# Optimization experiments

Measured on AMD Instinct MI355X. Metric: run time of the kernel, lower is better.

## Reference

```python
import jax, jax.numpy as jnp
import numpy as np

B, S, D = 8, 2048, 256


def setup_inputs() -> dict:
    key = jax.random.key(0)
    k1, k2, k3, k4, k5 = jax.random.split(key, 5)
    head = jax.random.normal(k1, (B, S, D), dtype=jnp.float32)
    dep = jax.random.normal(k2, (B, S, D), dtype=jnp.float32)
    edge_U = jax.random.normal(k3, (D, D), dtype=jnp.float32) / np.sqrt(D)
    edge_W = jax.random.normal(k4, (1, 2 * D), dtype=jnp.float32) / np.sqrt(2 * D)
    edge_b = jax.random.normal(k5, (1,), dtype=jnp.float32)
    return {"head": head, "dep": dep, "edge_U": edge_U, "edge_W": edge_W, "edge_b": edge_b}


def reference(head, dep, edge_U, edge_W, edge_b):
    # t1[b,i,o] = head[b,i,:] @ U @ dep[b,o,:]  -> [B,S,S]
    t1 = jnp.einsum('bid,de,boe->bio', head, edge_U, dep)
    # t2: linear over pairwise concat(head_i, dep_o); decomposes into two
    # broadcast-added matvecs (same math as W @ concat, no [B,S^2,2D] tensor).
    d = head.shape[-1]
    wh, wd = edge_W[0, :d], edge_W[0, d:]
    hs = head @ wh  # [B,S]
    ds = dep @ wd   # [B,S]
    t2 = hs[:, :, None] + ds[:, None, :]  # [B,S,S]
    return t1 + t2 + edge_b[0]
```

## Files before the change

kernel.cpp:

```cpp
#include <hip/hip_runtime.h>
#include <hip/hip_bf16.h>
#include <stdint.h>
#include <stddef.h>

#define B_ 8
#define S_ 2048
#define D_ 256
#define NROWS (B_ * S_)

typedef __attribute__((ext_vector_type(8))) short short8;
typedef __attribute__((ext_vector_type(4))) short short4v;
typedef __attribute__((ext_vector_type(4))) float f32x4;

__device__ __forceinline__ short bf16of(float f) {
  union { float f; unsigned u; } x; x.f = f;
  unsigned r = x.u + 0x7FFFu + ((x.u >> 16) & 1u);
  return (short)(r >> 16);
}

__device__ __forceinline__ void async_ld16(const void* g, void* s) {
  __builtin_amdgcn_global_load_lds(
      (const __attribute__((address_space(1))) void*)g,
      (__attribute__((address_space(3))) void*)s, 16, 0, 0);
}

__global__ void k_prep_u(const float* __restrict__ U, short* __restrict__ UT) {
  int n = blockIdx.x;
  int k = threadIdx.x;
  UT[n * D_ + k] = bf16of(U[k * D_ + n]);
}

__global__ void k_rows(const float* __restrict__ head, const float* __restrict__ dep,
                       const float* __restrict__ W,
                       float* __restrict__ hs, float* __restrict__ ds,
                       short* __restrict__ headB, short* __restrict__ depB) {
  const float* X; const float* wv; float* sv; short* XB;
  if (blockIdx.y == 0) { X = head; wv = W;      sv = hs; XB = headB; }
  else                 { X = dep;  wv = W + D_; sv = ds; XB = depB;  }
  const int row = blockIdx.x * 4 + (threadIdx.x >> 6);
  const int l = threadIdx.x & 63;
  const float4 v  = *(const float4*)(X + (size_t)row * D_ + l * 4);
  const float4 wq = *(const float4*)(wv + l * 4);
  short4v pk;
  pk[0] = bf16of(v.x); pk[1] = bf16of(v.y); pk[2] = bf16of(v.z); pk[3] = bf16of(v.w);
  *(short4v*)(XB + (size_t)row * D_ + l * 4) = pk;
  float p = v.x * wq.x + v.y * wq.y + v.z * wq.z + v.w * wq.w;
  p += __shfl_xor(p, 1); p += __shfl_xor(p, 2); p += __shfl_xor(p, 4);
  p += __shfl_xor(p, 8); p += __shfl_xor(p, 16); p += __shfl_xor(p, 32);
  if (l == 0) sv[row] = p;
}

__launch_bounds__(256, 2)
__global__ void k_ahat(const short* __restrict__ headB, const short* __restrict__ UT,
                       short* __restrict__ Ahat) {
  __shared__ __align__(16) short sU[4 * 128 * 32];
  __shared__ __align__(16) short sH[4 * 128 * 32];
  const int t = threadIdx.x;
  const int w = t >> 6;
  const int l = t & 63;
  const int quad = l >> 4;
  const int nbase = blockIdx.x * 128;
  const int mbase = blockIdx.y * 128;

  f32x4 acc[4][4];
#pragma unroll
  for (int i = 0; i < 4; ++i)
#pragma unroll
    for (int j = 0; j < 4; ++j) acc[i][j] = (f32x4)0.0f;

  for (int it = 0; it < 2; ++it) {
    __syncthreads();
#pragma unroll
    for (int kb = 0; kb < 4; ++kb) {
#pragma unroll
      for (int c = 0; c < 2; ++c) {
        int q = c * 256 + t;
        int r = q >> 2, qc = q & 3;
        int kk = it * 128 + kb * 32 + qc * 8;
        async_ld16(UT + (size_t)(nbase + r) * D_ + kk, (char*)sU + kb * 8192 + q * 16);
        async_ld16(headB + (size_t)(mbase + r) * D_ + kk, (char*)sH + kb * 8192 + q * 16);
      }
    }
    __syncthreads();
    const short8* pU = (const short8*)sU;
    const short8* pH = (const short8*)sH;
#pragma unroll
    for (int kb = 0; kb < 4; ++kb) {
      short8 aF[4], bF[4];
#pragma unroll
      for (int mt = 0; mt < 4; ++mt)
        aF[mt] = pU[(kb * 128 + (w >> 1) * 64 + mt * 16 + (l & 15)) * 4 + quad];
#pragma unroll
      for (int nt = 0; nt < 4; ++nt)
        bF[nt] = pH[(kb * 128 + (w & 1) * 64 + nt * 16 + (l & 15)) * 4 + quad];
#pragma unroll
      for (int mt = 0; mt < 4; ++mt)
#pragma unroll
        for (int nt = 0; nt < 4; ++nt)
          acc[mt][nt] = __builtin_amdgcn_mfma_f32_16x16x32_bf16(aF[mt], bF[nt], acc[mt][nt], 0, 0, 0);
    }
  }

#pragma unroll
  for (int mt = 0; mt < 4; ++mt) {
    int n_loc = (w >> 1) * 64 + mt * 16 + quad * 4;
#pragma unroll
    for (int nt = 0; nt < 4; ++nt) {
      int i_loc = (w & 1) * 64 + nt * 16 + (l & 15);
      short4v pk;
      pk[0] = bf16of(acc[mt][nt][0]); pk[1] = bf16of(acc[mt][nt][1]);
      pk[2] = bf16of(acc[mt][nt][2]); pk[3] = bf16of(acc[mt][nt][3]);
      *(short4v*)(Ahat + (size_t)(mbase + i_loc) * D_ + nbase + n_loc) = pk;
    }
  }
}

__launch_bounds__(256, 3)
__global__ void k_main(const short* __restrict__ Ahat, const short* __restrict__ depB,
                       const float* __restrict__ hs, const float* __restrict__ ds,
                       const float* __restrict__ eb, float* __restrict__ out) {
  __shared__ __align__(16) short sA[2 * 128 * 32];
  __shared__ __align__(16) short sD[2 * 128 * 32];
  __shared__ float hs_s[128];
  __shared__ float ds_s[128];
  const int t = threadIdx.x;
  const int w = t >> 6;
  const int l = t & 63;
  const int quad = l >> 4;
  const int b = blockIdx.z;
  const int mbase = blockIdx.y * 128;
  const int nbase = blockIdx.x * 128;

  if (t < 128) hs_s[t] = hs[b * S_ + mbase + t];
  else         ds_s[t - 128] = ds[b * S_ + nbase + t - 128];

  f32x4 acc[4][4];
#pragma unroll
  for (int i = 0; i < 4; ++i)
#pragma unroll
    for (int j = 0; j < 4; ++j) acc[i][j] = (f32x4)0.0f;

  for (int it = 0; it < 4; ++it) {
    __syncthreads();
#pragma unroll
    for (int kb = 0; kb < 2; ++kb) {
#pragma unroll
      for (int c = 0; c < 2; ++c) {
        int q = c * 256 + t;
        int r = q >> 2, qc = q & 3;
        int kk = it * 64 + kb * 32 + qc * 8;
        async_ld16(Ahat + (size_t)(b * S_ + mbase + r) * D_ + kk, (char*)sA + kb * 8192 + q * 16);
        async_ld16(depB + (size_t)(b * S_ + nbase + r) * D_ + kk, (char*)sD + kb * 8192 + q * 16);
      }
    }
    __syncthreads();
    const short8* pA = (const short8*)sA;
    const short8* pD = (const short8*)sD;
#pragma unroll
    for (int kb = 0; kb < 2; ++kb) {
      short8 aF[4], bF[4];
#pragma unroll
      for (int mt = 0; mt < 4; ++mt)
        aF[mt] = pD[(kb * 128 + (w >> 1) * 64 + mt * 16 + (l & 15)) * 4 + quad];
#pragma unroll
      for (int nt = 0; nt < 4; ++nt)
        bF[nt] = pA[(kb * 128 + (w & 1) * 64 + nt * 16 + (l & 15)) * 4 + quad];
#pragma unroll
      for (int mt = 0; mt < 4; ++mt)
#pragma unroll
        for (int nt = 0; nt < 4; ++nt)
          acc[mt][nt] = __builtin_amdgcn_mfma_f32_16x16x32_bf16(aF[mt], bF[nt], acc[mt][nt], 0, 0, 0);
    }
  }

  const float bias = eb[0];
#pragma unroll
  for (int mt = 0; mt < 4; ++mt) {
    int o_loc = (w >> 1) * 64 + mt * 16 + quad * 4;
    float4 dsv = *(const float4*)&ds_s[o_loc];
#pragma unroll
    for (int nt = 0; nt < 4; ++nt) {
      int i_loc = (w & 1) * 64 + nt * 16 + (l & 15);
      float hv = hs_s[i_loc] + bias;
      f32x4 a = acc[mt][nt];
      float4 o4;
      o4.x = a[0] + hv + dsv.x;
      o4.y = a[1] + hv + dsv.y;
      o4.z = a[2] + hv + dsv.z;
      o4.w = a[3] + hv + dsv.w;
      *(float4*)(out + (size_t)(b * S_ + mbase + i_loc) * S_ + nbase + o_loc) = o4;
    }
  }
}

extern "C" void kernel_launch(void* const* d_in, const int* in_sizes, int n_in,
                              void* d_out, int out_size, void* d_ws, size_t ws_size,
                              hipStream_t stream) {
  const float* head = (const float*)d_in[0];
  const float* dep  = (const float*)d_in[1];
  const float* U    = (const float*)d_in[2];
  const float* W    = (const float*)d_in[3];
  const float* eb   = (const float*)d_in[4];
  float* out = (float*)d_out;

  char* ws = (char*)d_ws;
  short* UT    = (short*)ws;
  float* hs    = (float*)(ws + (128 << 10));
  float* ds    = (float*)(ws + (192 << 10));
  short* headB = (short*)(ws + (256 << 10));
  short* depB  = (short*)(ws + (256 << 10) + (8 << 20));
  short* Ahat  = (short*)(ws + (256 << 10) + (16 << 20));

  k_prep_u<<<dim3(256), dim3(256), 0, stream>>>(U, UT);
  k_rows<<<dim3(NROWS / 4, 2), dim3(256), 0, stream>>>(head, dep, W, hs, ds, headB, depB);
  k_ahat<<<dim3(2, 128), dim3(256), 0, stream>>>(headB, UT, Ahat);
  k_main<<<dim3(16, 16, 8), dim3(256), 0, stream>>>(Ahat, depB, hs, ds, eb, out);
}
```

Baseline: 193.4 us.

## Load MFMA fragments directly from global memory instead of staging through LDS

Both GEMM kernels drop their LDS staging buffers and barriers. Each wave now loads its bf16 MFMA operand fragments straight from global memory (16-byte vector loads per lane) inside a K loop unrolled by two. The epilogue bias vectors are also read directly from global memory rather than shared memory, and k_ahat's occupancy hint goes from 2 to 3. This removes LDS traffic and synchronisation, but operands are no longer shared across the waves of a block, so each tile is fetched redundantly from L1/L2 with strided access.

```diff
diff --git a/kernel.cpp b/kernel.cpp
--- a/kernel.cpp
+++ b/kernel.cpp
@@ -16,12 +16,6 @@
   union { float f; unsigned u; } x; x.f = f;
   unsigned r = x.u + 0x7FFFu + ((x.u >> 16) & 1u);
   return (short)(r >> 16);
-}
-
-__device__ __forceinline__ void async_ld16(const void* g, void* s) {
-  __builtin_amdgcn_global_load_lds(
-      (const __attribute__((address_space(1))) void*)g,
-      (__attribute__((address_space(3))) void*)s, 16, 0, 0);
 }
 
 __global__ void k_prep_u(const float* __restrict__ U, short* __restrict__ UT) {
@@ -50,17 +44,19 @@
   if (l == 0) sv[row] = p;
 }
 
-__launch_bounds__(256, 2)
+__launch_bounds__(256, 3)
 __global__ void k_ahat(const short* __restrict__ headB, const short* __restrict__ UT,
                        short* __restrict__ Ahat) {
-  __shared__ __align__(16) short sU[4 * 128 * 32];
-  __shared__ __align__(16) short sH[4 * 128 * 32];
   const int t = threadIdx.x;
   const int w = t >> 6;
   const int l = t & 63;
   const int quad = l >> 4;
+  const int r15 = l & 15;
   const int nbase = blockIdx.x * 128;
   const int mbase = blockIdx.y * 128;
+
+  const short* pA = UT + (size_t)(nbase + (w >> 1) * 64 + r15) * D_ + quad * 8;
+  const short* pB = headB + (size_t)(mbase + (w & 1) * 64 + r15) * D_ + quad * 8;
 
   f32x4 acc[4][4];
 #pragma unroll
@@ -68,37 +64,20 @@
 #pragma unroll
     for (int j = 0; j < 4; ++j) acc[i][j] = (f32x4)0.0f;
 
-  for (int it = 0; it < 2; ++it) {
-    __syncthreads();
+#pragma unroll 2
+  for (int k0 = 0; k0 < D_; k0 += 32) {
+    short8 aF[4], bF[4];
 #pragma unroll
-    for (int kb = 0; kb < 4; ++kb) {
+    for (int mt = 0; mt < 4; ++mt)
+      aF[mt] = *(const short8*)(pA + (size_t)(mt * 16) * D_ + k0);
 #pragma unroll
-      for (int c = 0; c < 2; ++c) {
-        int q = c * 256 + t;
-        int r = q >> 2, qc = q & 3;
-        int kk = it * 128 + kb * 32 + qc * 8;
-        async_ld16(UT + (size_t)(nbase + r) * D_ + kk, (char*)sU + kb * 8192 + q * 16);
-        async_ld16(headB + (size_t)(mbase + r) * D_ + kk, (char*)sH + kb * 8192 + q * 16);
-      }
-    }
-    __syncthreads();
-    const short8* pU = (const short8*)sU;
-    const short8* pH = (const short8*)sH;
+    for (int nt = 0; nt < 4; ++nt)
+      bF[nt] = *(const short8*)(pB + (size_t)(nt * 16) * D_ + k0);
 #pragma unroll
-    for (int kb = 0; kb < 4; ++kb) {
-      short8 aF[4], bF[4];
-#pragma unroll
-      for (int mt = 0; mt < 4; ++mt)
-        aF[mt] = pU[(kb * 128 + (w >> 1) * 64 + mt * 16 + (l & 15)) * 4 + quad];
+    for (int mt = 0; mt < 4; ++mt)
 #pragma unroll
       for (int nt = 0; nt < 4; ++nt)
-        bF[nt] = pH[(kb * 128 + (w & 1) * 64 + nt * 16 + (l & 15)) * 4 + quad];
-#pragma unroll
-      for (int mt = 0; mt < 4; ++mt)
-#pragma unroll
-        for (int nt = 0; nt < 4; ++nt)
-          acc[mt][nt] = __builtin_amdgcn_mfma_f32_16x16x32_bf16(aF[mt], bF[nt], acc[mt][nt], 0, 0, 0);
-    }
+        acc[mt][nt] = __builtin_amdgcn_mfma_f32_16x16x32_bf16(aF[mt], bF[nt], acc[mt][nt], 0, 0, 0);
   }
 
 #pragma unroll
@@ -106,7 +85,7 @@
     int n_loc = (w >> 1) * 64 + mt * 16 + quad * 4;
 #pragma unroll
     for (int nt = 0; nt < 4; ++nt) {
-      int i_loc = (w & 1) * 64 + nt * 16 + (l & 15);
+      int i_loc = (w & 1) * 64 + nt * 16 + r15;
       short4v pk;
       pk[0] = bf16of(acc[mt][nt][0]); pk[1] = bf16of(acc[mt][nt][1]);
       pk[2] = bf16of(acc[mt][nt][2]); pk[3] = bf16of(acc[mt][nt][3]);
@@ -119,20 +98,17 @@
 __global__ void k_main(const short* __restrict__ Ahat, const short* __restrict__ depB,
                        const float* __restrict__ hs, const float* __restrict__ ds,
                        const float* __restrict__ eb, float* __restrict__ out) {
-  __shared__ __align__(16) short sA[2 * 128 * 32];
-  __shared__ __align__(16) short sD[2 * 128 * 32];
-  __shared__ float hs_s[128];
-  __shared__ float ds_s[128];
   const int t = threadIdx.x;
   const int w = t >> 6;
   const int l = t & 63;
   const int quad = l >> 4;
+  const int r15 = l & 15;
   const int b = blockIdx.z;
   const int mbase = blockIdx.y * 128;
   const int nbase = blockIdx.x * 128;
 
-  if (t < 128) hs_s[t] = hs[b * S_ + mbase + t];
-  else         ds_s[t - 128] = ds[b * S_ + nbase + t - 128];
+  const short* pA = depB + (size_t)(b * S_ + nbase + (w >> 1) * 64 + r15) * D_ + quad * 8;
+  const short* pB = Ahat + (size_t)(b * S_ + mbase + (w & 1) * 64 + r15) * D_ + quad * 8;
 
   f32x4 acc[4][4];
 #pragma unroll
@@ -140,48 +116,36 @@
 #pragma unroll
     for (int j = 0; j < 4; ++j) acc[i][j] = (f32x4)0.0f;
 
-  for (int it = 0; it < 4; ++it) {
-    __syncthreads();
+#pragma unroll 2
+  for (int k0 = 0; k0 < D_; k0 += 32) {
+    short8 aF[4], bF[4];
 #pragma unroll
-    for (int kb = 0; kb < 2; ++kb) {
+    for (int mt = 0; mt < 4; ++mt)
+      aF[mt] = *(const short8*)(pA + (size_t)(mt * 16) * D_ + k0);
 #pragma unroll
-      for (int c = 0; c < 2; ++c) {
-        int q = c * 256 + t;
-        int r = q >> 2, qc = q & 3;
-        int kk = it * 64 + kb * 32 + qc * 8;
-        async_ld16(Ahat + (size_t)(b * S_ + mbase + r) * D_ + kk, (char*)sA + kb * 8192 + q * 16);
-        async_ld16(depB + (size_t)(b * S_ + nbase + r) * D_ + kk, (char*)sD + kb * 8192 + q * 16);
-      }
-    }
-    __syncthreads();
-    const short8* pA = (const short8*)sA;
-    const short8* pD = (const short8*)sD;
+    for (int nt = 0; nt < 4; ++nt)
+      bF[nt] = *(const short8*)(pB + (size_t)(nt * 16) * D_ + k0);
 #pragma unroll
-    for (int kb = 0; kb < 2; ++kb) {
-      short8 aF[4], bF[4];
-#pragma unroll
-      for (int mt = 0; mt < 4; ++mt)
-        aF[mt] = pD[(kb * 128 + (w >> 1) * 64 + mt * 16 + (l & 15)) * 4 + quad];
+    for (int mt = 0; mt < 4; ++mt)
 #pragma unroll
       for (int nt = 0; nt < 4; ++nt)
-        bF[nt] = pA[(kb * 128 + (w & 1) * 64 + nt * 16 + (l & 15)) * 4 + quad];
-#pragma unroll
-      for (int mt = 0; mt < 4; ++mt)
-#pragma unroll
-        for (int nt = 0; nt < 4; ++nt)
-          acc[mt][nt] = __builtin_amdgcn_mfma_f32_16x16x32_bf16(aF[mt], bF[nt], acc[mt][nt], 0, 0, 0);
-    }
+        acc[mt][nt] = __builtin_amdgcn_mfma_f32_16x16x32_bf16(aF[mt], bF[nt], acc[mt][nt], 0, 0, 0);
   }
 
   const float bias = eb[0];
+  float hv4[4];
+#pragma unroll
+  for (int nt = 0; nt < 4; ++nt)
+    hv4[nt] = hs[(size_t)b * S_ + mbase + (w & 1) * 64 + nt * 16 + r15] + bias;
+
 #pragma unroll
   for (int mt = 0; mt < 4; ++mt) {
     int o_loc = (w >> 1) * 64 + mt * 16 + quad * 4;
-    float4 dsv = *(const float4*)&ds_s[o_loc];
+    float4 dsv = *(const float4*)(ds + (size_t)b * S_ + nbase + o_loc);
 #pragma unroll
     for (int nt = 0; nt < 4; ++nt) {
-      int i_loc = (w & 1) * 64 + nt * 16 + (l & 15);
-      float hv = hs_s[i_loc] + bias;
+      int i_loc = (w & 1) * 64 + nt * 16 + r15;
+      float hv = hv4[nt];
       f32x4 a = acc[mt][nt];
       float4 o4;
       o4.x = a[0] + hv + dsv.x;
```

Result: slower. 236.9 us (+22.5%).
